# Optimization experiments

Hardware: AMD Instinct MI355X
Metric: run time of the kernel (lower is better)

The kernel has to match this reference:

```python
import jax, jax.numpy as jnp
import numpy as np

N_NODES = 100000
N_EDGES = 1600000
IN_CH = 128
OUT_CH = 64
HID = 2 * OUT_CH  # 128


def _gcn_norm(edge_index, num_nodes):
    # add self-loops, compute symmetric normalization D^-1/2 (A+I) D^-1/2
    loops = jnp.arange(num_nodes, dtype=edge_index.dtype)
    src = jnp.concatenate([edge_index[0], loops])
    dst = jnp.concatenate([edge_index[1], loops])
    deg = jax.ops.segment_sum(jnp.ones_like(dst, dtype=jnp.float32), dst,
                              num_segments=num_nodes)
    dinv = jnp.where(deg > 0, jax.lax.rsqrt(deg), 0.0)
    norm = dinv[src] * dinv[dst]  # [E + N]
    return src, dst, norm


def _gcn_conv(x, W, b, src, dst, norm, num_nodes):
    h = x @ W                                   # [N, F_out]
    msg = h[src] * norm[:, None]                # gather + scale, [E+N, F_out]
    out = jax.ops.segment_sum(msg, dst, num_segments=num_nodes)
    return out + b


def setup_inputs() -> dict:
    key = jax.random.key(0)
    k1, k2, k3, k4 = jax.random.split(key, 4)
    x = jax.random.normal(k1, (N_NODES, IN_CH), dtype=jnp.float32)
    edge_index = jax.random.randint(k2, (2, N_EDGES), 0, N_NODES, dtype=jnp.int32)
    W1 = jax.random.normal(k3, (IN_CH, HID), dtype=jnp.float32) / np.sqrt(IN_CH)
    b1 = jnp.zeros((HID,), dtype=jnp.float32)
    W2 = jax.random.normal(k4, (HID, OUT_CH), dtype=jnp.float32) / np.sqrt(HID)
    b2 = jnp.zeros((OUT_CH,), dtype=jnp.float32)
    return {"x": x, "edge_index": edge_index, "W1": W1, "b1": b1,
            "W2": W2, "b2": b2}


def reference(x, edge_index, W1, b1, W2, b2):
    n = x.shape[0]
    src, dst, norm = _gcn_norm(edge_index, n)
    z = jax.nn.relu(_gcn_conv(x, W1, b1, src, dst, norm, n))
    return _gcn_conv(z, W2, b2, src, dst, norm, n)
```

## Files before the change

kernel.cpp:

```cpp
#include <hip/hip_runtime.h>

#define DEV_INLINE __device__ __forceinline__

static constexpr int KDIM = 128;
static constexpr int BUCKET_SHIFT = 8;
static constexpr int BUCKET_NODES = 1 << BUCKET_SHIFT;
static constexpr int CAP = 6144;
static constexpr int MAXNB = 512;

using s16x8 = __attribute__((ext_vector_type(8))) short;
using f32x4 = __attribute__((ext_vector_type(4))) float;

DEV_INLINE float bf2f_lo(unsigned int u) {
    union { unsigned int u; float f; } c; c.u = u << 16; return c.f;
}
DEV_INLINE unsigned int f2bf(float f) {
    union { float f; unsigned int u; } c; c.f = f;
    return (c.u + 0x7FFFu + ((c.u >> 16) & 1u)) >> 16;
}

DEV_INLINE void fma8(float w, const uint4& h, float* acc) {
    acc[0] = fmaf(w, bf2f_lo(h.x), acc[0]);
    acc[1] = fmaf(w, bf2f_lo(h.x >> 16), acc[1]);
    acc[2] = fmaf(w, bf2f_lo(h.y), acc[2]);
    acc[3] = fmaf(w, bf2f_lo(h.y >> 16), acc[3]);
    acc[4] = fmaf(w, bf2f_lo(h.z), acc[4]);
    acc[5] = fmaf(w, bf2f_lo(h.z >> 16), acc[5]);
    acc[6] = fmaf(w, bf2f_lo(h.w), acc[6]);
    acc[7] = fmaf(w, bf2f_lo(h.w >> 16), acc[7]);
}

__global__ void k_zero(int* __restrict__ bucket_cursor, int nb) {
    int i = blockIdx.x * 256 + threadIdx.x;
    if (i < nb) bucket_cursor[i] = 0;
}

template <int EPT>
__global__ __launch_bounds__(256) void k_bin(
    const int* __restrict__ src, const int* __restrict__ dst,
    int* __restrict__ bucket_cursor, unsigned int* __restrict__ rec,
    int E, int NB) {
    __shared__ int hist[MAXNB];
    __shared__ int base[MAXNB];
    const int t = threadIdx.x;
    for (int i = t; i < NB; i += 256) hist[i] = 0;
    __syncthreads();

    const int e0 = blockIdx.x * (256 * EPT);
    int d[EPT], s[EPT];
#pragma unroll
    for (int i = 0; i < EPT; ++i) {
        int e = e0 + i * 256 + t;
        d[i] = (e < E) ? dst[e] : -1;
        s[i] = (e < E) ? src[e] : 0;
    }
#pragma unroll
    for (int i = 0; i < EPT; ++i)
        if (d[i] >= 0) atomicAdd(&hist[d[i] >> BUCKET_SHIFT], 1);
    __syncthreads();

    for (int i = t; i < NB; i += 256) {
        int h = hist[i];
        base[i] = (h > 0) ? atomicAdd(&bucket_cursor[i], h) : 0;
        hist[i] = 0;
    }
    __syncthreads();

#pragma unroll
    for (int i = 0; i < EPT; ++i) {
        if (d[i] >= 0) {
            int b = d[i] >> BUCKET_SHIFT;
            int r = atomicAdd(&hist[b], 1);
            unsigned int p = (unsigned int)s[i] |
                             ((unsigned int)(d[i] & (BUCKET_NODES - 1)) << 24);
            rec[(size_t)b * CAP + base[b] + r] = p;
        }
    }
}

__global__ __launch_bounds__(256) void k_degcsr(
    const int* __restrict__ bucket_cursor, const unsigned int* __restrict__ rec,
    int* __restrict__ csr_src, int* __restrict__ row_start, int* __restrict__ row_end,
    float* __restrict__ dinv, int N) {
    __shared__ int cnt[BUCKET_NODES];
    __shared__ int rstart[BUCKET_NODES];
    __shared__ int sc[BUCKET_NODES];
    const int b = blockIdx.x;
    const int t = threadIdx.x;
    const int node0 = b << BUCKET_SHIFT;
    const int ne = bucket_cursor[b];
    cnt[t] = 0;
    __syncthreads();

    const unsigned int* r0 = rec + (size_t)b * CAP;
    for (int j = t; j < ne; j += 256) atomicAdd(&cnt[r0[j] >> 24], 1);
    __syncthreads();

    int v = cnt[t];
    sc[t] = v;
    __syncthreads();
    for (int off = 1; off < 256; off <<= 1) {
        int add = (t >= off) ? sc[t - off] : 0;
        __syncthreads();
        sc[t] += add;
        __syncthreads();
    }
    int rs = sc[t] - v;
    rstart[t] = rs;
    if (node0 + t < N) {
        row_start[node0 + t] = b * CAP + rs;
        row_end[node0 + t]   = b * CAP + rs + v;
        dinv[node0 + t] = rsqrtf((float)v + 1.0f);
    }
    cnt[t] = 0;
    __syncthreads();

    for (int j = t; j < ne; j += 256) {
        unsigned int p = r0[j];
        int loc = p >> 24;
        int rk = atomicAdd(&cnt[loc], 1);
        csr_src[(size_t)b * CAP + rstart[loc] + rk] = (int)(p & 0x00FFFFFFu);
    }
}

__global__ void k_wprep(const float* __restrict__ W, unsigned short* __restrict__ Wf,
                        int NOUT) {
    const int tid = blockIdx.x * 256 + threadIdx.x;
    const int CT = NOUT >> 4;
    const int total = 8 * CT * 64;
    if (tid >= total) return;
    const int lane = tid & 63;
    const int f = tid >> 6;
    const int v = f / (4 * CT);
    const int r = f - v * 4 * CT;
    const int s = r / CT;
    const int ct = r - s * CT;
    const int k0 = s * 32 + ((lane >> 4) << 3);
    const int n = (ct << 4) + (lane & 15);
    unsigned int pk[4];
#pragma unroll
    for (int jp = 0; jp < 4; ++jp) {
        unsigned int h2[2];
#pragma unroll
        for (int e = 0; e < 2; ++e) {
            int j = jp * 2 + e;
            float w = W[(size_t)(k0 + j) * NOUT + n];
            unsigned int hb = f2bf(w);
            if (v) hb = f2bf(w - bf2f_lo(hb));
            h2[e] = hb;
        }
        pk[jp] = h2[0] | (h2[1] << 16);
    }
    reinterpret_cast<uint4*>(Wf)[tid] = make_uint4(pk[0], pk[1], pk[2], pk[3]);
}

template <int NOUT, bool RELU_IN>
__global__ __launch_bounds__(256, 2) void k_mgemm(
    const float* __restrict__ A, const unsigned short* __restrict__ Wf,
    const float* __restrict__ dinv,
    unsigned short* __restrict__ Hs, int N) {
    constexpr int CT = NOUT / 16;
    constexpr int U4 = CT * 512;
    __shared__ uint4 WfL[U4];
    for (int i = threadIdx.x; i < U4; i += 256)
        WfL[i] = reinterpret_cast<const uint4*>(Wf)[i];
    __syncthreads();

    const int lane = threadIdx.x & 63;
    const int kg = lane >> 4;
    const int lm = lane & 15;
    const int r0 = blockIdx.x * 64 + (threadIdx.x >> 6) * 16;
    const int arow = r0 + lm;

    s16x8 ah[4], al[4];
    const float4* A4 = reinterpret_cast<const float4*>(A);
#pragma unroll
    for (int s = 0; s < 4; ++s) {
        float4 p0 = make_float4(0.f, 0.f, 0.f, 0.f);
        float4 p1 = p0;
        if (arow < N) {
            p0 = A4[(size_t)arow * 32 + s * 8 + kg * 2];
            p1 = A4[(size_t)arow * 32 + s * 8 + kg * 2 + 1];
        }
        float vf[8] = {p0.x, p0.y, p0.z, p0.w, p1.x, p1.y, p1.z, p1.w};
#pragma unroll
        for (int j = 0; j < 8; ++j) {
            float w = RELU_IN ? fmaxf(vf[j], 0.f) : vf[j];
            unsigned int hb = f2bf(w);
            ah[s][j] = (short)hb;
            al[s][j] = (short)f2bf(w - bf2f_lo(hb));
        }
    }

    float dv[4];
#pragma unroll
    for (int q = 0; q < 4; ++q) {
        int orow = r0 + kg * 4 + q;
        dv[q] = (orow < N) ? dinv[orow] : 0.f;
    }

    const unsigned short* LW = reinterpret_cast<const unsigned short*>(WfL);
#pragma unroll
    for (int ct = 0; ct < CT; ++ct) {
        f32x4 acc = {0.f, 0.f, 0.f, 0.f};
#pragma unroll
        for (int s = 0; s < 4; ++s) {
            s16x8 bh = *reinterpret_cast<const s16x8*>(LW + ((size_t)(s * CT + ct)) * 512 + lane * 8);
            s16x8 bl = *reinterpret_cast<const s16x8*>(LW + ((size_t)((4 + s) * CT + ct)) * 512 + lane * 8);
            acc = __builtin_amdgcn_mfma_f32_16x16x32_bf16(ah[s], bh, acc, 0, 0, 0);
            acc = __builtin_amdgcn_mfma_f32_16x16x32_bf16(al[s], bh, acc, 0, 0, 0);
            acc = __builtin_amdgcn_mfma_f32_16x16x32_bf16(ah[s], bl, acc, 0, 0, 0);
        }
        const int col = ct * 16 + lm;
#pragma unroll
        for (int q = 0; q < 4; ++q) {
            int orow = r0 + kg * 4 + q;
            if (orow < N)
                Hs[(size_t)orow * NOUT + col] = (unsigned short)f2bf(dv[q] * acc[q]);
        }
    }
}

template <int NOUT>
__global__ void k_gather(const int* __restrict__ row_start, const int* __restrict__ row_end,
                         const int* __restrict__ csr_src,
                         const float* __restrict__ dinv,
                         const unsigned short* __restrict__ Hs,
                         const float* __restrict__ bias,
                         float* __restrict__ Out, int N) {
    constexpr int LPG = NOUT / 8;
    const int lane = threadIdx.x % LPG;
    const int node = blockIdx.x * (256 / LPG) + threadIdx.x / LPG;
    if (node >= N) return;
    const int s0 = row_start[node];
    const int s1 = row_end[node];
    const float dn = dinv[node];
    const uint4* H8 = reinterpret_cast<const uint4*>(Hs);
    float acc[8];
#pragma unroll
    for (int i = 0; i < 8; ++i) acc[i] = 0.f;

    int j = s0;
    for (; j + 2 <= s1; j += 2) {
        int sa = csr_src[j];
        int sb = csr_src[j + 1];
        uint4 ha = H8[(size_t)sa * LPG + lane];
        uint4 hb = H8[(size_t)sb * LPG + lane];
        fma8(dn, ha, acc);
        fma8(dn, hb, acc);
    }
    if (j < s1) {
        int sa = csr_src[j];
        uint4 ha = H8[(size_t)sa * LPG + lane];
        fma8(dn, ha, acc);
    }
    {
        uint4 hv = H8[(size_t)node * LPG + lane];
        fma8(dn, hv, acc);
    }

    const float4* B4 = reinterpret_cast<const float4*>(bias + lane * 8);
    float4 b0 = B4[0], b1 = B4[1];
    float4 o0, o1;
    o0.x = acc[0] + b0.x; o0.y = acc[1] + b0.y; o0.z = acc[2] + b0.z; o0.w = acc[3] + b0.w;
    o1.x = acc[4] + b1.x; o1.y = acc[5] + b1.y; o1.z = acc[6] + b1.z; o1.w = acc[7] + b1.w;
    float4* O4 = reinterpret_cast<float4*>(Out + (size_t)node * NOUT + lane * 8);
    O4[0] = o0; O4[1] = o1;
}

extern "C" void kernel_launch(void* const* d_in, const int* in_sizes, int n_in,
                              void* d_out, int out_size, void* d_ws, size_t ws_size,
                              hipStream_t stream) {
    const float* x  = (const float*)d_in[0];
    const int*   ei = (const int*)d_in[1];
    const float* W1 = (const float*)d_in[2];
    const float* b1 = (const float*)d_in[3];
    const float* W2 = (const float*)d_in[4];
    const float* b2 = (const float*)d_in[5];
    float* out = (float*)d_out;

    const int N = in_sizes[0] / 128;
    const int E = in_sizes[1] / 2;
    const int* src = ei;
    const int* dst = ei + E;
    const int NB = (N + BUCKET_NODES - 1) >> BUCKET_SHIFT;

    char* ws = (char*)d_ws;
    size_t off = 0;
    auto alloc = [&](size_t bytes) -> char* {
        char* p = ws + off;
        off += (bytes + 255) & ~size_t(255);
        return p;
    };
    int*            bucket_cursor = (int*)alloc((size_t)MAXNB * 4);
    int*            row_start     = (int*)alloc((size_t)N * 4);
    int*            row_end       = (int*)alloc((size_t)N * 4);
    float*          dinv          = (float*)alloc((size_t)N * 4);
    unsigned int*   rec           = (unsigned int*)alloc((size_t)NB * CAP * 4);
    int*            csr_src       = (int*)alloc((size_t)NB * CAP * 4);
    unsigned short* hs1           = (unsigned short*)alloc((size_t)N * 128 * 2);
    unsigned short* hs2           = (unsigned short*)alloc((size_t)N * 64 * 2);
    float*          zp            = (float*)alloc((size_t)N * 128 * 4);
    unsigned short* wf1           = (unsigned short*)alloc(128 * 128 * 2 * 2);
    unsigned short* wf2           = (unsigned short*)alloc(128 * 64 * 2 * 2);
    (void)ws_size; (void)n_in; (void)out_size;

    constexpr int EPT = 8;
    const int bin_blocks = (E + 256 * EPT - 1) / (256 * EPT);

    hipLaunchKernelGGL(k_zero, dim3((NB + 255) / 256), dim3(256), 0, stream,
                       bucket_cursor, NB);
    hipLaunchKernelGGL(k_wprep, dim3(16), dim3(256), 0, stream, W1, wf1, 128);
    hipLaunchKernelGGL(k_wprep, dim3(8), dim3(256), 0, stream, W2, wf2, 64);
    hipLaunchKernelGGL((k_bin<EPT>), dim3(bin_blocks), dim3(256), 0, stream,
                       src, dst, bucket_cursor, rec, E, NB);
    hipLaunchKernelGGL(k_degcsr, dim3(NB), dim3(256), 0, stream,
                       bucket_cursor, rec, csr_src, row_start, row_end, dinv, N);

    hipLaunchKernelGGL((k_mgemm<128, false>), dim3((N + 63) / 64), dim3(256), 0, stream,
                       x, wf1, dinv, hs1, N);

    hipLaunchKernelGGL((k_gather<128>), dim3((N + 15) / 16), dim3(256), 0, stream,
                       row_start, row_end, csr_src, dinv, hs1, b1, zp, N);

    hipLaunchKernelGGL((k_mgemm<64, true>), dim3((N + 63) / 64), dim3(256), 0, stream,
                       zp, wf2, dinv, hs2, N);

    hipLaunchKernelGGL((k_gather<64>), dim3((N + 31) / 32), dim3(256), 0, stream,
                       row_start, row_end, csr_src, dinv, hs2, b2, out, N);
}
```

Measured before the change: 298.6 us.

## Store layer-1 features as FP8 and hidden activations as bf16 with fused ReLU

Layer-1 transformed features are now written as FP8 (one byte per value) instead of bf16, which halves the bytes moved by the first random-access gather. The first gather now applies bias and ReLU and writes the hidden activations as bf16 instead of fp32. The second GEMM therefore reads bf16 directly and drops the low-part split term. Both gathers unroll the edge loop by four. This cuts memory traffic in the bandwidth-bound gather and GEMM stages, but FP8 storage adds sizeable quantisation error that may exceed the accuracy tolerance.

```diff
diff --git a/kernel.cpp b/kernel.cpp
--- a/kernel.cpp
+++ b/kernel.cpp
@@ -10,6 +10,7 @@
 
 using s16x8 = __attribute__((ext_vector_type(8))) short;
 using f32x4 = __attribute__((ext_vector_type(4))) float;
+using f32x2 = __attribute__((ext_vector_type(2))) float;
 
 DEV_INLINE float bf2f_lo(unsigned int u) {
     union { unsigned int u; float f; } c; c.u = u << 16; return c.f;
@@ -28,6 +29,26 @@
     acc[5] = fmaf(w, bf2f_lo(h.z >> 16), acc[5]);
     acc[6] = fmaf(w, bf2f_lo(h.w), acc[6]);
     acc[7] = fmaf(w, bf2f_lo(h.w >> 16), acc[7]);
+}
+
+DEV_INLINE void fma4fp8(float w, unsigned int u, float* acc) {
+    f32x2 p;
+    p = __builtin_amdgcn_cvt_pk_f32_fp8((int)u, false);
+    acc[0] = fmaf(w, p[0], acc[0]);
+    acc[1] = fmaf(w, p[1], acc[1]);
+    p = __builtin_amdgcn_cvt_pk_f32_fp8((int)u, true);
+    acc[2] = fmaf(w, p[0], acc[2]);
+    acc[3] = fmaf(w, p[1], acc[3]);
+}
+DEV_INLINE void fma16fp8(float w, const uint4& h, float* acc) {
+    fma4fp8(w, h.x, acc);
+    fma4fp8(w, h.y, acc + 4);
+    fma4fp8(w, h.z, acc + 8);
+    fma4fp8(w, h.w, acc + 12);
+}
+
+DEV_INLINE unsigned char f2fp8(float f) {
+    return (unsigned char)(__builtin_amdgcn_cvt_pk_fp8_f32(f, f, 0, false) & 0xFF);
 }
 
 __global__ void k_zero(int* __restrict__ bucket_cursor, int nb) {
@@ -154,12 +175,11 @@
     reinterpret_cast<uint4*>(Wf)[tid] = make_uint4(pk[0], pk[1], pk[2], pk[3]);
 }
 
-template <int NOUT, bool RELU_IN>
-__global__ __launch_bounds__(256, 2) void k_mgemm(
+__global__ __launch_bounds__(256, 2) void k_mgemm1(
     const float* __restrict__ A, const unsigned short* __restrict__ Wf,
     const float* __restrict__ dinv,
-    unsigned short* __restrict__ Hs, int N) {
-    constexpr int CT = NOUT / 16;
+    unsigned char* __restrict__ Hs, int N) {
+    constexpr int CT = 8;
     constexpr int U4 = CT * 512;
     __shared__ uint4 WfL[U4];
     for (int i = threadIdx.x; i < U4; i += 256)
@@ -185,10 +205,9 @@
         float vf[8] = {p0.x, p0.y, p0.z, p0.w, p1.x, p1.y, p1.z, p1.w};
 #pragma unroll
         for (int j = 0; j < 8; ++j) {
-            float w = RELU_IN ? fmaxf(vf[j], 0.f) : vf[j];
-            unsigned int hb = f2bf(w);
+            unsigned int hb = f2bf(vf[j]);
             ah[s][j] = (short)hb;
-            al[s][j] = (short)f2bf(w - bf2f_lo(hb));
+            al[s][j] = (short)f2bf(vf[j] - bf2f_lo(hb));
         }
     }
 
@@ -216,21 +235,127 @@
         for (int q = 0; q < 4; ++q) {
             int orow = r0 + kg * 4 + q;
             if (orow < N)
-                Hs[(size_t)orow * NOUT + col] = (unsigned short)f2bf(dv[q] * acc[q]);
-        }
-    }
-}
-
-template <int NOUT>
-__global__ void k_gather(const int* __restrict__ row_start, const int* __restrict__ row_end,
-                         const int* __restrict__ csr_src,
-                         const float* __restrict__ dinv,
-                         const unsigned short* __restrict__ Hs,
-                         const float* __restrict__ bias,
-                         float* __restrict__ Out, int N) {
-    constexpr int LPG = NOUT / 8;
-    const int lane = threadIdx.x % LPG;
-    const int node = blockIdx.x * (256 / LPG) + threadIdx.x / LPG;
+                Hs[(size_t)orow * 128 + col] = f2fp8(dv[q] * acc[q]);
+        }
+    }
+}
+
+__global__ __launch_bounds__(256, 4) void k_mgemm2(
+    const unsigned short* __restrict__ Z, const unsigned short* __restrict__ Wf,
+    const float* __restrict__ dinv,
+    unsigned short* __restrict__ Hs, int N) {
+    constexpr int CT = 4;
+    constexpr int U4 = CT * 512;
+    __shared__ uint4 WfL[U4];
+    for (int i = threadIdx.x; i < U4; i += 256)
+        WfL[i] = reinterpret_cast<const uint4*>(Wf)[i];
+    __syncthreads();
+
+    const int lane = threadIdx.x & 63;
+    const int kg = lane >> 4;
+    const int lm = lane & 15;
+    const int r0 = blockIdx.x * 64 + (threadIdx.x >> 6) * 16;
+    const int arow = r0 + lm;
+
+    s16x8 ah[4];
+    const s16x8* Z8 = reinterpret_cast<const s16x8*>(Z);
+#pragma unroll
+    for (int s = 0; s < 4; ++s) {
+        if (arow < N) ah[s] = Z8[(size_t)arow * 16 + s * 4 + kg];
+        else          ah[s] = s16x8{0, 0, 0, 0, 0, 0, 0, 0};
+    }
+
+    float dv[4];
+#pragma unroll
+    for (int q = 0; q < 4; ++q) {
+        int orow = r0 + kg * 4 + q;
+        dv[q] = (orow < N) ? dinv[orow] : 0.f;
+    }
+
+    const unsigned short* LW = reinterpret_cast<const unsigned short*>(WfL);
+#pragma unroll
+    for (int ct = 0; ct < CT; ++ct) {
+        f32x4 acc = {0.f, 0.f, 0.f, 0.f};
+#pragma unroll
+        for (int s = 0; s < 4; ++s) {
+            s16x8 bh = *reinterpret_cast<const s16x8*>(LW + ((size_t)(s * CT + ct)) * 512 + lane * 8);
+            s16x8 bl = *reinterpret_cast<const s16x8*>(LW + ((size_t)((4 + s) * CT + ct)) * 512 + lane * 8);
+            acc = __builtin_amdgcn_mfma_f32_16x16x32_bf16(ah[s], bh, acc, 0, 0, 0);
+            acc = __builtin_amdgcn_mfma_f32_16x16x32_bf16(ah[s], bl, acc, 0, 0, 0);
+        }
+        const int col = ct * 16 + lm;
+#pragma unroll
+        for (int q = 0; q < 4; ++q) {
+            int orow = r0 + kg * 4 + q;
+            if (orow < N)
+                Hs[(size_t)orow * 64 + col] = (unsigned short)f2bf(dv[q] * acc[q]);
+        }
+    }
+}
+
+__global__ void k_gather1(const int* __restrict__ row_start, const int* __restrict__ row_end,
+                          const int* __restrict__ csr_src,
+                          const float* __restrict__ dinv,
+                          const unsigned char* __restrict__ Hs,
+                          const float* __restrict__ b1,
+                          unsigned short* __restrict__ Zp, int N) {
+    const int lane = threadIdx.x & 7;
+    const int node = blockIdx.x * 32 + (threadIdx.x >> 3);
+    if (node >= N) return;
+    const int s0 = row_start[node];
+    const int s1 = row_end[node];
+    const float dn = dinv[node];
+    const uint4* H = reinterpret_cast<const uint4*>(Hs);
+    float acc[16];
+#pragma unroll
+    for (int i = 0; i < 16; ++i) acc[i] = 0.f;
+
+    int j = s0;
+    for (; j + 4 <= s1; j += 4) {
+        int sa = csr_src[j], sb = csr_src[j + 1], sc = csr_src[j + 2], sd = csr_src[j + 3];
+        uint4 ha = H[(size_t)sa * 8 + lane];
+        uint4 hb = H[(size_t)sb * 8 + lane];
+        uint4 hc = H[(size_t)sc * 8 + lane];
+        uint4 hd = H[(size_t)sd * 8 + lane];
+        fma16fp8(dn, ha, acc);
+        fma16fp8(dn, hb, acc);
+        fma16fp8(dn, hc, acc);
+        fma16fp8(dn, hd, acc);
+    }
+    for (; j < s1; ++j) {
+        uint4 h = H[(size_t)csr_src[j] * 8 + lane];
+        fma16fp8(dn, h, acc);
+    }
+    {
+        uint4 h = H[(size_t)node * 8 + lane];
+        fma16fp8(dn, h, acc);
+    }
+
+    const float4* B4 = reinterpret_cast<const float4*>(b1 + lane * 16);
+    unsigned int pk[8];
+#pragma unroll
+    for (int p = 0; p < 4; ++p) {
+        float4 b = B4[p];
+        float f0 = fmaxf(acc[p * 4 + 0] + b.x, 0.f);
+        float f1 = fmaxf(acc[p * 4 + 1] + b.y, 0.f);
+        float f2 = fmaxf(acc[p * 4 + 2] + b.z, 0.f);
+        float f3 = fmaxf(acc[p * 4 + 3] + b.w, 0.f);
+        pk[p * 2]     = f2bf(f0) | (f2bf(f1) << 16);
+        pk[p * 2 + 1] = f2bf(f2) | (f2bf(f3) << 16);
+    }
+    uint4* O = reinterpret_cast<uint4*>(Zp + (size_t)node * 128 + lane * 16);
+    O[0] = make_uint4(pk[0], pk[1], pk[2], pk[3]);
+    O[1] = make_uint4(pk[4], pk[5], pk[6], pk[7]);
+}
+
+__global__ void k_gather2(const int* __restrict__ row_start, const int* __restrict__ row_end,
+                          const int* __restrict__ csr_src,
+                          const float* __restrict__ dinv,
+                          const unsigned short* __restrict__ Hs,
+                          const float* __restrict__ b2,
+                          float* __restrict__ Out, int N) {
+    const int lane = threadIdx.x & 7;
+    const int node = blockIdx.x * 32 + (threadIdx.x >> 3);
     if (node >= N) return;
     const int s0 = row_start[node];
     const int s1 = row_end[node];
@@ -241,30 +366,32 @@
     for (int i = 0; i < 8; ++i) acc[i] = 0.f;
 
     int j = s0;
-    for (; j + 2 <= s1; j += 2) {
-        int sa = csr_src[j];
-        int sb = csr_src[j + 1];
-        uint4 ha = H8[(size_t)sa * LPG + lane];
-        uint4 hb = H8[(size_t)sb * LPG + lane];
+    for (; j + 4 <= s1; j += 4) {
+        int sa = csr_src[j], sb = csr_src[j + 1], sc = csr_src[j + 2], sd = csr_src[j + 3];
+        uint4 ha = H8[(size_t)sa * 8 + lane];
+        uint4 hb = H8[(size_t)sb * 8 + lane];
+        uint4 hc = H8[(size_t)sc * 8 + lane];
+        uint4 hd = H8[(size_t)sd * 8 + lane];
         fma8(dn, ha, acc);
         fma8(dn, hb, acc);
-    }
-    if (j < s1) {
-        int sa = csr_src[j];
-        uint4 ha = H8[(size_t)sa * LPG + lane];
-        fma8(dn, ha, acc);
+        fma8(dn, hc, acc);
+        fma8(dn, hd, acc);
+    }
+    for (; j < s1; ++j) {
+        uint4 h = H8[(size_t)csr_src[j] * 8 + lane];
+        fma8(dn, h, acc);
     }
     {
-        uint4 hv = H8[(size_t)node * LPG + lane];
-        fma8(dn, hv, acc);
-    }
-
-    const float4* B4 = reinterpret_cast<const float4*>(bias + lane * 8);
-    float4 b0 = B4[0], b1 = B4[1];
+        uint4 h = H8[(size_t)node * 8 + lane];
+        fma8(dn, h, acc);
+    }
+
+    const float4* B4 = reinterpret_cast<const float4*>(b2 + lane * 8);
+    float4 b0 = B4[0], b1v = B4[1];
     float4 o0, o1;
-    o0.x = acc[0] + b0.x; o0.y = acc[1] + b0.y; o0.z = acc[2] + b0.z; o0.w = acc[3] + b0.w;
-    o1.x = acc[4] + b1.x; o1.y = acc[5] + b1.y; o1.z = acc[6] + b1.z; o1.w = acc[7] + b1.w;
-    float4* O4 = reinterpret_cast<float4*>(Out + (size_t)node * NOUT + lane * 8);
+    o0.x = acc[0] + b0.x;  o0.y = acc[1] + b0.y;  o0.z = acc[2] + b0.z;  o0.w = acc[3] + b0.w;
+    o1.x = acc[4] + b1v.x; o1.y = acc[5] + b1v.y; o1.z = acc[6] + b1v.z; o1.w = acc[7] + b1v.w;
+    float4* O4 = reinterpret_cast<float4*>(Out + (size_t)node * 64 + lane * 8);
     O4[0] = o0; O4[1] = o1;
 }
 
@@ -298,9 +425,9 @@
     float*          dinv          = (float*)alloc((size_t)N * 4);
     unsigned int*   rec           = (unsigned int*)alloc((size_t)NB * CAP * 4);
     int*            csr_src       = (int*)alloc((size_t)NB * CAP * 4);
-    unsigned short* hs1           = (unsigned short*)alloc((size_t)N * 128 * 2);
+    unsigned char*  hs1           = (unsigned char*)alloc((size_t)N * 128);
     unsigned short* hs2           = (unsigned short*)alloc((size_t)N * 64 * 2);
-    float*          zp            = (float*)alloc((size_t)N * 128 * 4);
+    unsigned short* zp            = (unsigned short*)alloc((size_t)N * 128 * 2);
     unsigned short* wf1           = (unsigned short*)alloc(128 * 128 * 2 * 2);
     unsigned short* wf2           = (unsigned short*)alloc(128 * 64 * 2 * 2);
     (void)ws_size; (void)n_in; (void)out_size;
@@ -317,15 +444,15 @@
     hipLaunchKernelGGL(k_degcsr, dim3(NB), dim3(256), 0, stream,
                        bucket_cursor, rec, csr_src, row_start, row_end, dinv, N);
 
-    hipLaunchKernelGGL((k_mgemm<128, false>), dim3((N + 63) / 64), dim3(256), 0, stream,
+    hipLaunchKernelGGL(k_mgemm1, dim3((N + 63) / 64), dim3(256), 0, stream,
                        x, wf1, dinv, hs1, N);
 
-    hipLaunchKernelGGL((k_gather<128>), dim3((N + 15) / 16), dim3(256), 0, stream,
+    hipLaunchKernelGGL(k_gather1, dim3((N + 31) / 32), dim3(256), 0, stream,
                        row_start, row_end, csr_src, dinv, hs1, b1, zp, N);
 
-    hipLaunchKernelGGL((k_mgemm<64, true>), dim3((N + 63) / 64), dim3(256), 0, stream,
+    hipLaunchKernelGGL(k_mgemm2, dim3((N + 63) / 64), dim3(256), 0, stream,
                        zp, wf2, dinv, hs2, N);
 
-    hipLaunchKernelGGL((k_gather<64>), dim3((N + 31) / 32), dim3(256), 0, stream,
+    hipLaunchKernelGGL(k_gather2, dim3((N + 31) / 32), dim3(256), 0, stream,
                        row_start, row_end, csr_src, dinv, hs2, b2, out, N);
 }
```

Result: faster. 261.5 us (median of 2 runs) (-12.4%).
